# Performance work log

Measured on AMD Instinct MI355X. Metric: run time of the kernel, lower is better.

The kernel has to match this reference:

```python
import jax, jax.numpy as jnp
import numpy as np

K, D = 1024, 256
B, H, W = 32, 32, 32


def setup_inputs() -> dict:
    key = jax.random.key(0)
    kx, kc = jax.random.split(key)
    x = jax.random.normal(kx, (B, D, H, W), dtype=jnp.float32)
    # nn.Embedding weight initialized uniform(-1/K, 1/K)
    codebook = jax.random.uniform(kc, (K, D), dtype=jnp.float32,
                                  minval=-1.0 / K, maxval=1.0 / K)
    return {"x": x, "codebook": codebook}


def reference(x, codebook):
    # x: [B, D, H, W] -> NHWC -> flatten to [N, D]
    xf = jnp.transpose(x, (0, 2, 3, 1)).reshape(-1, D)  # [N, D]
    # Squared Euclidean distances via ||a||^2 - 2 a.b + ||b||^2.
    # torch.cdist applies sqrt; sqrt is monotone so argmin over squared
    # distances yields identical indices without the extra elementwise pass.
    x_sq = jnp.sum(xf * xf, axis=1, keepdims=True)          # [N, 1]
    e_sq = jnp.sum(codebook * codebook, axis=1)             # [K]
    d2 = x_sq - 2.0 * (xf @ codebook.T) + e_sq              # [N, K]
    indices = jnp.argmin(d2, axis=1)                        # [N]
    return indices.reshape(B, H, W)
```

## Files before the change

kernel.cpp:

```cpp
#include <hip/hip_runtime.h>

#define K_CODES 1024
#define DIMS    256
#define NROWS   32768

typedef __attribute__((ext_vector_type(8))) short bf16x8;
typedef __attribute__((ext_vector_type(4))) float f32x4;


#define WS_BH    0
#define WS_ESQ   (WS_BH + 131072)
#define WS_CAND  (WS_ESQ + K_CODES)
#define WS_XP    (WS_CAND + NROWS * 8)
#define WS_MFMA_NEED_FLOATS (WS_XP + 3 * NROWS)
#define WS_MFMA_NEED_BYTES  ((size_t)WS_MFMA_NEED_FLOATS * 4)

#define F32_ET    0
#define F32_ESQ   (F32_ET  + DIMS * K_CODES)
#define F32_XSQ   (F32_ESQ + K_CODES)
#define F32_CAND  (F32_XSQ + NROWS)
#define F32_NEED_FLOATS (F32_CAND + 4 * NROWS * 2)
#define F32_NEED_BYTES  ((size_t)F32_NEED_FLOATS * 4)

__device__ __forceinline__ float sq_at(const float* p, int d, int stride) {
#pragma clang fp contract(off)
    const float v = p[(size_t)d * stride];
    return v * v;
}

__device__ __forceinline__ float np_block_sq(const float* p, int stride, int o, int n) {
#pragma clang fp contract(off)
    float r[8];
    #pragma unroll
    for (int k = 0; k < 8; ++k) r[k] = sq_at(p, o + k, stride);
    const int n8 = n - (n % 8);
    for (int i = 8; i < n8; i += 8) {
        #pragma unroll
        for (int k = 0; k < 8; ++k) r[k] = r[k] + sq_at(p, o + i + k, stride);
    }
    float res = ((r[0] + r[1]) + (r[2] + r[3])) + ((r[4] + r[5]) + (r[6] + r[7]));
    for (int i = n8; i < n; ++i) res = res + sq_at(p, o + i, stride);
    return res;
}

__device__ __forceinline__ float np_sumsq_row(const float* p, int stride) {
#pragma clang fp contract(off)
    const float p120 = np_block_sq(p, stride, 1,   120);
    const float p64  = np_block_sq(p, stride, 121, 64);
    const float p71  = np_block_sq(p, stride, 185, 71);
    const float s135 = p64 + p71;
    const float s255 = p120 + s135;
    return sq_at(p, 0, stride) + s255;
}

__device__ __forceinline__ unsigned short f32_to_bf16_rne(float f) {
    unsigned u = __float_as_uint(f);
    u += 0x7fffu + ((u >> 16) & 1u);
    return (unsigned short)(u >> 16);
}

__global__ void vq_prologue_mfma(const float* __restrict__ x, const float* __restrict__ cb,
                                 float* __restrict__ esq, unsigned short* __restrict__ bh,
                                 float* __restrict__ xp) {
    const int bid = blockIdx.x;
    if (bid < 4) {
        const int c = bid * 256 + threadIdx.x;
        esq[c] = np_sumsq_row(cb + (size_t)c * DIMS, 1);
    } else if (bid < 1028) {
        const int idx = (bid - 4) * 256 + threadIdx.x;
        const int i  = idx & 7;
        const int ln = (idx >> 3) & 63;
        const int t  = (idx >> 9) & 63;
        const int kc = idx >> 15;
        const int c  = t * 16 + (ln & 15);
        const int k  = kc * 32 + (ln >> 4) * 8 + i;
        bh[idx] = f32_to_bf16_rne(cb[(size_t)c * DIMS + k]);
    } else {
        const int bid2  = bid - 1028;
        const int piece = bid2 / 128;
        const int n     = (bid2 % 128) * 256 + threadIdx.x;
        const float* p  = x + ((size_t)(n >> 10)) * (DIMS * 1024) + (n & 1023);
        const int o   = (piece == 0) ? 1   : (piece == 1) ? 121 : 185;
        const int len = (piece == 0) ? 120 : (piece == 1) ? 64  : 71;
        xp[(size_t)piece * NROWS + n] = np_block_sq(p, 1024, o, len);
    }
}

__global__ __launch_bounds__(256, 2)
void vq_mfma_filter(const float* __restrict__ x, const unsigned short* __restrict__ bh,
                    const float* __restrict__ esq, int4* __restrict__ cand) {
    __shared__ int4 lbh[2][1024];

    const int tid  = (int)threadIdx.x;
    const int wid  = __builtin_amdgcn_readfirstlane(tid >> 6);
    const int lane = tid & 63;
    const int h      = blockIdx.x & 1;
    const int rowblk = (blockIdx.x >> 1) * 4 + wid;
    const int row0 = rowblk * 16;
    const int b  = row0 >> 10;
    const int hw = (row0 & 1023) + (lane & 15);
    const float* xb = x + (size_t)b * (DIMS * 1024) + hw;
    const int g = lane >> 4;
    const int tile0 = h * 32;

    bf16x8 afr[8];
    #pragma unroll
    for (int kc = 0; kc < 8; ++kc) {
        #pragma unroll
        for (int i = 0; i < 8; ++i) {
            const int k = kc * 32 + g * 8 + i;
            afr[kc][i] = (short)f32_to_bf16_rne(xb[(size_t)k * 1024]);
        }
    }

    float lv[4][2]; int lc[4][2];
    #pragma unroll
    for (int j = 0; j < 4; ++j) {
        lv[j][0] = 3.4e38f; lv[j][1] = 3.4e38f;
        lc[j][0] = 0x7fffffff; lc[j][1] = 0x7fffffff;
    }

    const int4* bh4 = reinterpret_cast<const int4*>(bh);

#define STAGE(BUF, CHUNK)                                                      \
    do {                                                                       \
        _Pragma("unroll")                                                      \
        for (int e = 0; e < 4; ++e) {                                          \
            const int idx = e * 256 + tid;                        \
            const int ln_ = idx & 63;                                          \
            const int tt_ = (idx >> 6) & 1;                                    \
            const int kc_ = idx >> 7;                                          \
            lbh[BUF][idx] =                                                    \
                bh4[(kc_ * 64 + tile0 + (CHUNK) * 2 + tt_) * 64 + ln_];        \
        }                                                                      \
    } while (0)

    STAGE(0, 0);
    __syncthreads();
    for (int chunk = 0; chunk < 16; ++chunk) {
        const int cur = chunk & 1;
        if (chunk + 1 < 16) STAGE(cur ^ 1, chunk + 1);

        #pragma unroll
        for (int tt = 0; tt < 2; ++tt) {
            const int t = tile0 + chunk * 2 + tt;
            f32x4 acch = {0.f, 0.f, 0.f, 0.f};
            #pragma unroll
            for (int kc = 0; kc < 8; ++kc) {
                const int li = (kc * 2 + tt) * 64 + lane;
                acch = __builtin_amdgcn_mfma_f32_16x16x32_bf16(
                    afr[kc], *reinterpret_cast<const bf16x8*>(&lbh[cur][li]), acch, 0, 0, 0);
            }
            const int   c  = t * 16 + (lane & 15);
            const float es = esq[c];
            #pragma unroll
            for (int j = 0; j < 4; ++j) {
                const float v = fmaf(-2.0f, acch[j], es);
                if (v < lv[j][0]) { lv[j][1] = lv[j][0]; lc[j][1] = lc[j][0]; lv[j][0] = v; lc[j][0] = c; }
                else if (v < lv[j][1]) { lv[j][1] = v; lc[j][1] = c; }
            }
        }
        __syncthreads();
    }
#undef STAGE

    int c3[4][3];
    #pragma unroll
    for (int j = 0; j < 4; ++j) {
        float a1v = lv[j][0]; int a1c = lc[j][0];
        float a2v = lv[j][1]; int a2c = lc[j][1];
        #pragma unroll
        for (int e = 0; e < 3; ++e) {
            float mv = a1v; int mc = a1c;
            #pragma unroll
            for (int off = 1; off < 16; off <<= 1) {
                const float ov = __shfl_xor(mv, off, 16);
                const int   oc = __shfl_xor(mc, off, 16);
                if (ov < mv || (ov == mv && oc < mc)) { mv = ov; mc = oc; }
            }
            c3[j][e] = mc;
            if (a1c == mc) { a1v = a2v; a1c = a2c; a2v = 3.4e38f; a2c = 0x7fffffff; }
        }
    }
    if ((lane & 15) == 0) {
        #pragma unroll
        for (int j = 0; j < 4; ++j)
            cand[(size_t)h * NROWS + row0 + g * 4 + j] =
                make_int4(c3[j][0], c3[j][1], c3[j][2], 0);
    }
}

__global__ __launch_bounds__(192, 2)
void vq_refine_fused(const float* __restrict__ x, const float* __restrict__ cb,
                     const float* __restrict__ esq, const int4* __restrict__ cand,
                     const float* __restrict__ xp, int* __restrict__ out) {
    __shared__ float sacc[6][32];
    __shared__ int   scc[6][32];

    const int t    = (int)threadIdx.x;
    const int r    = t & 31;
    const int slot = t >> 5;
    const int n  = blockIdx.x * 32 + r;
    const int b  = n >> 10;
    const int hw = n & 1023;
    const float* xr = x + (size_t)b * (DIMS * 1024) + hw;

    const int4 cd = cand[(size_t)(slot / 3) * NROWS + n];
    const int k3 = slot % 3;
    const int cc = (k3 == 0) ? cd.x : (k3 == 1) ? cd.y : cd.z;

    float acc = 0.f;
    for (int d0 = 0; d0 < DIMS; d0 += 32) {
        float xv[32];
        #pragma unroll
        for (int i = 0; i < 32; ++i) xv[i] = xr[(size_t)(d0 + i) * 1024];
        const float4* ec4 = reinterpret_cast<const float4*>(cb + (size_t)cc * DIMS + d0);
        #pragma unroll
        for (int q = 0; q < 8; ++q) {
            const float4 e = ec4[q];
            acc = fmaf(xv[q * 4 + 0], e.x, acc);
            acc = fmaf(xv[q * 4 + 1], e.y, acc);
            acc = fmaf(xv[q * 4 + 2], e.z, acc);
            acc = fmaf(xv[q * 4 + 3], e.w, acc);
        }
    }
    sacc[slot][r] = acc;
    scc[slot][r]  = cc;
    __syncthreads();
    if (t < 32) {
#pragma clang fp contract(off)
        const int n2  = blockIdx.x * 32 + t;
        const float x0 = x[(size_t)(n2 >> 10) * (DIMS * 1024) + (n2 & 1023)];
        const float q0 = x0 * x0;
        const float p120 = xp[n2];
        const float p64  = xp[NROWS + n2];
        const float p71  = xp[2 * NROWS + n2];
        const float s135 = p64 + p71;
        const float s255 = p120 + s135;
        const float xs   = q0 + s255;
        float bestv = 3.4e38f; int bestc = 0x7fffffff;
        #pragma unroll
        for (int k = 0; k < 6; ++k) {
            const float t3 = xs - 2.0f * sacc[k][t];
            const float v  = t3 + esq[scc[k][t]];
            if (v < bestv || (v == bestv && scc[k][t] < bestc)) { bestv = v; bestc = scc[k][t]; }
        }
        out[n2] = bestc;
    }
}

__global__ void vq_prologue_f32(const float* __restrict__ x, const float* __restrict__ cb,
                                float* __restrict__ xsq, float* __restrict__ esq,
                                float4* __restrict__ et4) {
    const int bid = blockIdx.x;
    if (bid < 128) {
        const int n = bid * 256 + threadIdx.x;
        const float* p = x + ((size_t)(n >> 10)) * (DIMS * 1024) + (n & 1023);
        xsq[n] = np_sumsq_row(p, 1024);
    } else if (bid < 132) {
        const int c = (bid - 128) * 256 + threadIdx.x;
        esq[c] = np_sumsq_row(cb + (size_t)c * DIMS, 1);
    } else {
        const int idx = (bid - 132) * 256 + threadIdx.x;
        const int dk  = idx & 63;
        const int c   = idx >> 6;
        const float4 v = *reinterpret_cast<const float4*>(cb + (size_t)c * DIMS + dk * 4);
        et4[(size_t)dk * K_CODES + c] = v;
    }
}

__global__ __launch_bounds__(256, 2)
void vq_main7_kernel(const float* __restrict__ x, const float4* __restrict__ et4,
                     const float* __restrict__ esq, const float* __restrict__ xsq,
                     float2* __restrict__ cand) {
    const int wid  = __builtin_amdgcn_readfirstlane((int)(threadIdx.x >> 6));
    const int lane = threadIdx.x & 63;
    const int W     = blockIdx.x * 4 + wid;
    const int g     = W & 3;
    const int slice = W >> 2;
    const int c0    = g * 256 + lane;
    const int row_base = slice * 8;
    const int b    = row_base >> 10;
    const int hw0  = row_base & 1023;
    const float* xb = x + (size_t)b * (DIMS * 1024) + hw0;

    const float esq0 = esq[c0];
    const float esq1 = esq[c0 + 64];
    const float esq2 = esq[c0 + 128];
    const float esq3 = esq[c0 + 192];

    float acc0[8], acc1[8], acc2[8], acc3[8];
    #pragma unroll
    for (int r = 0; r < 8; ++r) { acc0[r] = 0.0f; acc1[r] = 0.0f; acc2[r] = 0.0f; acc3[r] = 0.0f; }

    for (int dk = 0; dk < DIMS / 4; ++dk) {
        const float4* ep = et4 + (size_t)dk * K_CODES;
        const float4 e0 = ep[c0];
        const float4 e1 = ep[c0 + 64];
        const float4 e2 = ep[c0 + 128];
        const float4 e3 = ep[c0 + 192];

        #pragma unroll
        for (int dd = 0; dd < 4; ++dd) {
            float xv[8];
            #pragma unroll
            for (int r = 0; r < 8; ++r)
                xv[r] = xb[(size_t)(dk * 4 + dd) * 1024 + r];
            const float ev0 = (dd == 0) ? e0.x : (dd == 1) ? e0.y : (dd == 2) ? e0.z : e0.w;
            const float ev1 = (dd == 0) ? e1.x : (dd == 1) ? e1.y : (dd == 2) ? e1.z : e1.w;
            const float ev2 = (dd == 0) ? e2.x : (dd == 1) ? e2.y : (dd == 2) ? e2.z : e2.w;
            const float ev3 = (dd == 0) ? e3.x : (dd == 1) ? e3.y : (dd == 2) ? e3.z : e3.w;
            #pragma unroll
            for (int r = 0; r < 8; ++r) acc0[r] = fmaf(xv[r], ev0, acc0[r]);
            #pragma unroll
            for (int r = 0; r < 8; ++r) acc1[r] = fmaf(xv[r], ev1, acc1[r]);
            #pragma unroll
            for (int r = 0; r < 8; ++r) acc2[r] = fmaf(xv[r], ev2, acc2[r]);
            #pragma unroll
            for (int r = 0; r < 8; ++r) acc3[r] = fmaf(xv[r], ev3, acc3[r]);
        }
    }

    {
#pragma clang fp contract(off)
        float keepv = 0.0f; int keepc = 0;
        #pragma unroll
        for (int r = 0; r < 8; ++r) {
            const float xs_r = xsq[row_base + r];
            const float v0 = (xs_r - 2.0f * acc0[r]) + esq0;
            const float v1 = (xs_r - 2.0f * acc1[r]) + esq1;
            const float v2 = (xs_r - 2.0f * acc2[r]) + esq2;
            const float v3 = (xs_r - 2.0f * acc3[r]) + esq3;
            float bv = v0; int bc = c0;
            if (v1 < bv) { bv = v1; bc = c0 + 64; }
            if (v2 < bv) { bv = v2; bc = c0 + 128; }
            if (v3 < bv) { bv = v3; bc = c0 + 192; }
            #pragma unroll
            for (int off = 1; off < 64; off <<= 1) {
                const float ov = __shfl_xor(bv, off, 64);
                const int   oc = __shfl_xor(bc, off, 64);
                if (ov < bv || (ov == bv && oc < bc)) { bv = ov; bc = oc; }
            }
            if (lane == r) { keepv = bv; keepc = bc; }
        }
        if (lane < 8) {
            cand[(size_t)g * NROWS + row_base + lane] =
                make_float2(keepv, __int_as_float(keepc));
        }
    }
}

__global__ void vq_reduce_kernel(const float2* __restrict__ cand, int* __restrict__ out) {
    const int row = blockIdx.x * 256 + threadIdx.x;
    float2 p = cand[row];
    float bv = p.x; int bc = __float_as_int(p.y);
    #pragma unroll
    for (int gg = 1; gg < 4; ++gg) {
        const float2 q = cand[(size_t)gg * NROWS + row];
        const float v = q.x; const int qc = __float_as_int(q.y);
        if (v < bv || (v == bv && qc < bc)) { bv = v; bc = qc; }
    }
    out[row] = bc;
}

extern "C" void kernel_launch(void* const* d_in, const int* in_sizes, int n_in,
                              void* d_out, int out_size, void* d_ws, size_t ws_size,
                              hipStream_t stream) {
    const float* x  = (const float*)d_in[0];
    const float* cb = (const float*)d_in[1];
    int* out = (int*)d_out;
    float* ws = (float*)d_ws;

    if (ws_size >= WS_MFMA_NEED_BYTES) {
        unsigned short* bh = (unsigned short*)(ws + WS_BH);
        float* esq = ws + WS_ESQ;
        int4*  cnd = (int4*)(ws + WS_CAND);
        float* xp  = ws + WS_XP;

        vq_prologue_mfma<<<4 + 1024 + 384, 256, 0, stream>>>(x, cb, esq, bh, xp);
        vq_mfma_filter<<<1024, 256, 0, stream>>>(x, bh, esq, cnd);
        vq_refine_fused<<<NROWS / 32, 192, 0, stream>>>(x, cb, esq, cnd, xp, out);
        return;
    }
    {
        float4* et4  = (float4*)(ws + F32_ET);
        float*  esq  = ws + F32_ESQ;
        float*  xsq  = ws + F32_XSQ;
        float2* cand = (float2*)(ws + F32_CAND);

        vq_prologue_f32<<<128 + 4 + 256, 256, 0, stream>>>(x, cb, xsq, esq, et4);
        vq_main7_kernel<<<(NROWS / 8) * 4 / 4, 256, 0, stream>>>(x, et4, esq, xsq, cand);
        vq_reduce_kernel<<<NROWS / 256, 256, 0, stream>>>(cand, out);
    }
}
```

Measured before the change: 95.75 us.

## Split codebook into quarters, process two row groups per wave, keep top-2 candidates

The MFMA filter now gives each wave 32 rows (two 16-row A fragments) and a quarter of the codebook, so every staged B fragment from LDS feeds two MFMAs and codebook staging traffic per row is halved. Each quarter keeps top-2 candidates instead of each half keeping top-3, giving 8 candidates per row for the exact fp32 refine instead of 6. The refine kernel grows to 256 threads to rescore the 8 candidates. This raises register pressure in the filter (two A fragment sets and two accumulators) and increases refine work, while the candidate coverage changes and may affect correctness near ties.

```diff
diff --git a/kernel.cpp b/kernel.cpp
--- a/kernel.cpp
+++ b/kernel.cpp
@@ -88,37 +88,41 @@
 
 __global__ __launch_bounds__(256, 2)
 void vq_mfma_filter(const float* __restrict__ x, const unsigned short* __restrict__ bh,
-                    const float* __restrict__ esq, int4* __restrict__ cand) {
+                    const float* __restrict__ esq, int2* __restrict__ cand) {
     __shared__ int4 lbh[2][1024];
 
     const int tid  = (int)threadIdx.x;
     const int wid  = __builtin_amdgcn_readfirstlane(tid >> 6);
     const int lane = tid & 63;
-    const int h      = blockIdx.x & 1;
-    const int rowblk = (blockIdx.x >> 1) * 4 + wid;
-    const int row0 = rowblk * 16;
+    const int q      = blockIdx.x & 3;
+    const int rowblk = (blockIdx.x >> 2) * 4 + wid;
+    const int row0 = rowblk * 32;
     const int b  = row0 >> 10;
     const int hw = (row0 & 1023) + (lane & 15);
-    const float* xb = x + (size_t)b * (DIMS * 1024) + hw;
+    const float* xb0 = x + (size_t)b * (DIMS * 1024) + hw;
+    const float* xb1 = xb0 + 16;
     const int g = lane >> 4;
-    const int tile0 = h * 32;
-
-    bf16x8 afr[8];
+    const int tile0 = q * 16;
+
+    bf16x8 afr0[8], afr1[8];
     #pragma unroll
     for (int kc = 0; kc < 8; ++kc) {
         #pragma unroll
         for (int i = 0; i < 8; ++i) {
             const int k = kc * 32 + g * 8 + i;
-            afr[kc][i] = (short)f32_to_bf16_rne(xb[(size_t)k * 1024]);
-        }
-    }
-
-    float lv[4][2]; int lc[4][2];
-    #pragma unroll
-    for (int j = 0; j < 4; ++j) {
-        lv[j][0] = 3.4e38f; lv[j][1] = 3.4e38f;
-        lc[j][0] = 0x7fffffff; lc[j][1] = 0x7fffffff;
-    }
+            afr0[kc][i] = (short)f32_to_bf16_rne(xb0[(size_t)k * 1024]);
+            afr1[kc][i] = (short)f32_to_bf16_rne(xb1[(size_t)k * 1024]);
+        }
+    }
+
+    float lv[2][4][2]; int lc[2][4][2];
+    #pragma unroll
+    for (int rg = 0; rg < 2; ++rg)
+        #pragma unroll
+        for (int j = 0; j < 4; ++j) {
+            lv[rg][j][0] = 3.4e38f; lv[rg][j][1] = 3.4e38f;
+            lc[rg][j][0] = 0x7fffffff; lc[rg][j][1] = 0x7fffffff;
+        }
 
     const int4* bh4 = reinterpret_cast<const int4*>(bh);
 
@@ -137,65 +141,73 @@
 
     STAGE(0, 0);
     __syncthreads();
-    for (int chunk = 0; chunk < 16; ++chunk) {
+    for (int chunk = 0; chunk < 8; ++chunk) {
         const int cur = chunk & 1;
-        if (chunk + 1 < 16) STAGE(cur ^ 1, chunk + 1);
+        if (chunk + 1 < 8) STAGE(cur ^ 1, chunk + 1);
 
         #pragma unroll
         for (int tt = 0; tt < 2; ++tt) {
             const int t = tile0 + chunk * 2 + tt;
-            f32x4 acch = {0.f, 0.f, 0.f, 0.f};
+            f32x4 acc0 = {0.f, 0.f, 0.f, 0.f};
+            f32x4 acc1 = {0.f, 0.f, 0.f, 0.f};
             #pragma unroll
             for (int kc = 0; kc < 8; ++kc) {
                 const int li = (kc * 2 + tt) * 64 + lane;
-                acch = __builtin_amdgcn_mfma_f32_16x16x32_bf16(
-                    afr[kc], *reinterpret_cast<const bf16x8*>(&lbh[cur][li]), acch, 0, 0, 0);
+                const bf16x8 bf = *reinterpret_cast<const bf16x8*>(&lbh[cur][li]);
+                acc0 = __builtin_amdgcn_mfma_f32_16x16x32_bf16(afr0[kc], bf, acc0, 0, 0, 0);
+                acc1 = __builtin_amdgcn_mfma_f32_16x16x32_bf16(afr1[kc], bf, acc1, 0, 0, 0);
             }
             const int   c  = t * 16 + (lane & 15);
             const float es = esq[c];
             #pragma unroll
             for (int j = 0; j < 4; ++j) {
-                const float v = fmaf(-2.0f, acch[j], es);
-                if (v < lv[j][0]) { lv[j][1] = lv[j][0]; lc[j][1] = lc[j][0]; lv[j][0] = v; lc[j][0] = c; }
-                else if (v < lv[j][1]) { lv[j][1] = v; lc[j][1] = c; }
+                const float v0 = fmaf(-2.0f, acc0[j], es);
+                if (v0 < lv[0][j][0]) { lv[0][j][1] = lv[0][j][0]; lc[0][j][1] = lc[0][j][0]; lv[0][j][0] = v0; lc[0][j][0] = c; }
+                else if (v0 < lv[0][j][1]) { lv[0][j][1] = v0; lc[0][j][1] = c; }
+                const float v1 = fmaf(-2.0f, acc1[j], es);
+                if (v1 < lv[1][j][0]) { lv[1][j][1] = lv[1][j][0]; lc[1][j][1] = lc[1][j][0]; lv[1][j][0] = v1; lc[1][j][0] = c; }
+                else if (v1 < lv[1][j][1]) { lv[1][j][1] = v1; lc[1][j][1] = c; }
             }
         }
         __syncthreads();
     }
 #undef STAGE
 
-    int c3[4][3];
-    #pragma unroll
-    for (int j = 0; j < 4; ++j) {
-        float a1v = lv[j][0]; int a1c = lc[j][0];
-        float a2v = lv[j][1]; int a2c = lc[j][1];
-        #pragma unroll
-        for (int e = 0; e < 3; ++e) {
-            float mv = a1v; int mc = a1c;
-            #pragma unroll
-            for (int off = 1; off < 16; off <<= 1) {
-                const float ov = __shfl_xor(mv, off, 16);
-                const int   oc = __shfl_xor(mc, off, 16);
-                if (ov < mv || (ov == mv && oc < mc)) { mv = ov; mc = oc; }
+    #pragma unroll
+    for (int rg = 0; rg < 2; ++rg) {
+        int c2[4][2];
+        #pragma unroll
+        for (int j = 0; j < 4; ++j) {
+            float a1v = lv[rg][j][0]; int a1c = lc[rg][j][0];
+            float a2v = lv[rg][j][1]; int a2c = lc[rg][j][1];
+            #pragma unroll
+            for (int e = 0; e < 2; ++e) {
+                float mv = a1v; int mc = a1c;
+                #pragma unroll
+                for (int off = 1; off < 16; off <<= 1) {
+                    const float ov = __shfl_xor(mv, off, 16);
+                    const int   oc = __shfl_xor(mc, off, 16);
+                    if (ov < mv || (ov == mv && oc < mc)) { mv = ov; mc = oc; }
+                }
+                c2[j][e] = mc;
+                if (a1c == mc) { a1v = a2v; a1c = a2c; a2v = 3.4e38f; a2c = 0x7fffffff; }
             }
-            c3[j][e] = mc;
-            if (a1c == mc) { a1v = a2v; a1c = a2c; a2v = 3.4e38f; a2c = 0x7fffffff; }
-        }
-    }
-    if ((lane & 15) == 0) {
-        #pragma unroll
-        for (int j = 0; j < 4; ++j)
-            cand[(size_t)h * NROWS + row0 + g * 4 + j] =
-                make_int4(c3[j][0], c3[j][1], c3[j][2], 0);
-    }
-}
-
-__global__ __launch_bounds__(192, 2)
+        }
+        if ((lane & 15) == 0) {
+            #pragma unroll
+            for (int j = 0; j < 4; ++j)
+                cand[(size_t)q * NROWS + row0 + rg * 16 + g * 4 + j] =
+                    make_int2(c2[j][0], c2[j][1]);
+        }
+    }
+}
+
+__global__ __launch_bounds__(256, 2)
 void vq_refine_fused(const float* __restrict__ x, const float* __restrict__ cb,
-                     const float* __restrict__ esq, const int4* __restrict__ cand,
+                     const float* __restrict__ esq, const int2* __restrict__ cand,
                      const float* __restrict__ xp, int* __restrict__ out) {
-    __shared__ float sacc[6][32];
-    __shared__ int   scc[6][32];
+    __shared__ float sacc[8][32];
+    __shared__ int   scc[8][32];
 
     const int t    = (int)threadIdx.x;
     const int r    = t & 31;
@@ -205,9 +217,8 @@
     const int hw = n & 1023;
     const float* xr = x + (size_t)b * (DIMS * 1024) + hw;
 
-    const int4 cd = cand[(size_t)(slot / 3) * NROWS + n];
-    const int k3 = slot % 3;
-    const int cc = (k3 == 0) ? cd.x : (k3 == 1) ? cd.y : cd.z;
+    const int2 cd = cand[(size_t)(slot >> 1) * NROWS + n];
+    const int cc = (slot & 1) ? cd.y : cd.x;
 
     float acc = 0.f;
     for (int d0 = 0; d0 < DIMS; d0 += 32) {
@@ -216,12 +227,12 @@
         for (int i = 0; i < 32; ++i) xv[i] = xr[(size_t)(d0 + i) * 1024];
         const float4* ec4 = reinterpret_cast<const float4*>(cb + (size_t)cc * DIMS + d0);
         #pragma unroll
-        for (int q = 0; q < 8; ++q) {
-            const float4 e = ec4[q];
-            acc = fmaf(xv[q * 4 + 0], e.x, acc);
-            acc = fmaf(xv[q * 4 + 1], e.y, acc);
-            acc = fmaf(xv[q * 4 + 2], e.z, acc);
-            acc = fmaf(xv[q * 4 + 3], e.w, acc);
+        for (int qq = 0; qq < 8; ++qq) {
+            const float4 e = ec4[qq];
+            acc = fmaf(xv[qq * 4 + 0], e.x, acc);
+            acc = fmaf(xv[qq * 4 + 1], e.y, acc);
+            acc = fmaf(xv[qq * 4 + 2], e.z, acc);
+            acc = fmaf(xv[qq * 4 + 3], e.w, acc);
         }
     }
     sacc[slot][r] = acc;
@@ -240,7 +251,7 @@
         const float xs   = q0 + s255;
         float bestv = 3.4e38f; int bestc = 0x7fffffff;
         #pragma unroll
-        for (int k = 0; k < 6; ++k) {
+        for (int k = 0; k < 8; ++k) {
             const float t3 = xs - 2.0f * sacc[k][t];
             const float v  = t3 + esq[scc[k][t]];
             if (v < bestv || (v == bestv && scc[k][t] < bestc)) { bestv = v; bestc = scc[k][t]; }
@@ -374,12 +385,12 @@
     if (ws_size >= WS_MFMA_NEED_BYTES) {
         unsigned short* bh = (unsigned short*)(ws + WS_BH);
         float* esq = ws + WS_ESQ;
-        int4*  cnd = (int4*)(ws + WS_CAND);
+        int2*  cnd = (int2*)(ws + WS_CAND);
         float* xp  = ws + WS_XP;
 
         vq_prologue_mfma<<<4 + 1024 + 384, 256, 0, stream>>>(x, cb, esq, bh, xp);
         vq_mfma_filter<<<1024, 256, 0, stream>>>(x, bh, esq, cnd);
-        vq_refine_fused<<<NROWS / 32, 192, 0, stream>>>(x, cb, esq, cnd, xp, out);
+        vq_refine_fused<<<NROWS / 32, 256, 0, stream>>>(x, cb, esq, cnd, xp, out);
         return;
     }
     {
```

New measurement: 114.3 us. 19.3% more time.

## Switch filter kernel to 32x32x16 bf16 MFMA tiles with 32-row waves

Applied to the files above, without the earlier changes.

The filter kernel moves from 16x16x32 MFMA to 32x32x16 MFMA. Each wave now covers 32 rows instead of 16, and each tile covers 32 codes. The codebook bf16 layout and the LDS staging are reorganized to match, and the block count is halved. The larger tile reuses each A and B fragment over more outputs per instruction, lowering LDS traffic per flop. In exchange it raises register pressure (16 A fragments, 16x2 top-2 trackers, a 16-float accumulator) and lengthens the cross-lane reductions to 32 lanes.

```diff
diff --git a/kernel.cpp b/kernel.cpp
--- a/kernel.cpp
+++ b/kernel.cpp
@@ -4,8 +4,8 @@
 #define DIMS    256
 #define NROWS   32768
 
-typedef __attribute__((ext_vector_type(8))) short bf16x8;
-typedef __attribute__((ext_vector_type(4))) float f32x4;
+typedef __attribute__((ext_vector_type(8)))  short bf16x8;
+typedef __attribute__((ext_vector_type(16))) float f32x16;
 
 
 #define WS_BH    0
@@ -68,12 +68,12 @@
         esq[c] = np_sumsq_row(cb + (size_t)c * DIMS, 1);
     } else if (bid < 1028) {
         const int idx = (bid - 4) * 256 + threadIdx.x;
-        const int i  = idx & 7;
-        const int ln = (idx >> 3) & 63;
-        const int t  = (idx >> 9) & 63;
-        const int kc = idx >> 15;
-        const int c  = t * 16 + (ln & 15);
-        const int k  = kc * 32 + (ln >> 4) * 8 + i;
+        const int i    = idx & 7;
+        const int ln   = (idx >> 3) & 63;
+        const int tile = (idx >> 9) & 31;
+        const int kc   = idx >> 14;
+        const int c = tile * 32 + (ln & 31);
+        const int k = kc * 16 + (ln >> 5) * 8 + i;
         bh[idx] = f32_to_bf16_rne(cb[(size_t)c * DIMS + k]);
     } else {
         const int bid2  = bid - 1028;
@@ -96,97 +96,89 @@
     const int lane = tid & 63;
     const int h      = blockIdx.x & 1;
     const int rowblk = (blockIdx.x >> 1) * 4 + wid;
-    const int row0 = rowblk * 16;
+    const int row0 = rowblk * 32;
     const int b  = row0 >> 10;
-    const int hw = (row0 & 1023) + (lane & 15);
+    const int hw = (row0 & 1023) + (lane & 31);
     const float* xb = x + (size_t)b * (DIMS * 1024) + hw;
-    const int g = lane >> 4;
-    const int tile0 = h * 32;
-
-    bf16x8 afr[8];
-    #pragma unroll
-    for (int kc = 0; kc < 8; ++kc) {
+    const int tile0 = h * 16;
+
+    bf16x8 afr[16];
+    #pragma unroll
+    for (int kc = 0; kc < 16; ++kc) {
         #pragma unroll
         for (int i = 0; i < 8; ++i) {
-            const int k = kc * 32 + g * 8 + i;
+            const int k = kc * 16 + (lane >> 5) * 8 + i;
             afr[kc][i] = (short)f32_to_bf16_rne(xb[(size_t)k * 1024]);
         }
     }
 
-    float lv[4][2]; int lc[4][2];
-    #pragma unroll
-    for (int j = 0; j < 4; ++j) {
-        lv[j][0] = 3.4e38f; lv[j][1] = 3.4e38f;
-        lc[j][0] = 0x7fffffff; lc[j][1] = 0x7fffffff;
+    float lv[16][2]; int lc[16][2];
+    #pragma unroll
+    for (int r = 0; r < 16; ++r) {
+        lv[r][0] = 3.4e38f; lv[r][1] = 3.4e38f;
+        lc[r][0] = 0x7fffffff; lc[r][1] = 0x7fffffff;
     }
 
     const int4* bh4 = reinterpret_cast<const int4*>(bh);
 
-#define STAGE(BUF, CHUNK)                                                      \
+#define STAGE(BUF, TILE)                                                       \
     do {                                                                       \
         _Pragma("unroll")                                                      \
         for (int e = 0; e < 4; ++e) {                                          \
             const int idx = e * 256 + tid;                        \
             const int ln_ = idx & 63;                                          \
-            const int tt_ = (idx >> 6) & 1;                                    \
-            const int kc_ = idx >> 7;                                          \
-            lbh[BUF][idx] =                                                    \
-                bh4[(kc_ * 64 + tile0 + (CHUNK) * 2 + tt_) * 64 + ln_];        \
+            const int kc_ = idx >> 6;                               \
+            lbh[BUF][idx] = bh4[(kc_ * 32 + (TILE)) * 64 + ln_];               \
         }                                                                      \
     } while (0)
 
-    STAGE(0, 0);
+    STAGE(0, tile0);
     __syncthreads();
-    for (int chunk = 0; chunk < 16; ++chunk) {
-        const int cur = chunk & 1;
-        if (chunk + 1 < 16) STAGE(cur ^ 1, chunk + 1);
-
-        #pragma unroll
-        for (int tt = 0; tt < 2; ++tt) {
-            const int t = tile0 + chunk * 2 + tt;
-            f32x4 acch = {0.f, 0.f, 0.f, 0.f};
-            #pragma unroll
-            for (int kc = 0; kc < 8; ++kc) {
-                const int li = (kc * 2 + tt) * 64 + lane;
-                acch = __builtin_amdgcn_mfma_f32_16x16x32_bf16(
-                    afr[kc], *reinterpret_cast<const bf16x8*>(&lbh[cur][li]), acch, 0, 0, 0);
-            }
-            const int   c  = t * 16 + (lane & 15);
-            const float es = esq[c];
-            #pragma unroll
-            for (int j = 0; j < 4; ++j) {
-                const float v = fmaf(-2.0f, acch[j], es);
-                if (v < lv[j][0]) { lv[j][1] = lv[j][0]; lc[j][1] = lc[j][0]; lv[j][0] = v; lc[j][0] = c; }
-                else if (v < lv[j][1]) { lv[j][1] = v; lc[j][1] = c; }
-            }
+    for (int t = 0; t < 16; ++t) {
+        const int cur = t & 1;
+        if (t + 1 < 16) STAGE(cur ^ 1, tile0 + t + 1);
+
+        f32x16 acc = {0.f, 0.f, 0.f, 0.f, 0.f, 0.f, 0.f, 0.f,
+                      0.f, 0.f, 0.f, 0.f, 0.f, 0.f, 0.f, 0.f};
+        #pragma unroll
+        for (int kc = 0; kc < 16; ++kc) {
+            const int li = kc * 64 + lane;
+            acc = __builtin_amdgcn_mfma_f32_32x32x16_bf16(
+                afr[kc], *reinterpret_cast<const bf16x8*>(&lbh[cur][li]), acc, 0, 0, 0);
+        }
+        const int   c  = (tile0 + t) * 32 + (lane & 31);
+        const float es = esq[c];
+        #pragma unroll
+        for (int r = 0; r < 16; ++r) {
+            const float v = fmaf(-2.0f, acc[r], es);
+            if (v < lv[r][0]) { lv[r][1] = lv[r][0]; lc[r][1] = lc[r][0]; lv[r][0] = v; lc[r][0] = c; }
+            else if (v < lv[r][1]) { lv[r][1] = v; lc[r][1] = c; }
         }
         __syncthreads();
     }
 #undef STAGE
 
-    int c3[4][3];
-    #pragma unroll
-    for (int j = 0; j < 4; ++j) {
-        float a1v = lv[j][0]; int a1c = lc[j][0];
-        float a2v = lv[j][1]; int a2c = lc[j][1];
+    #pragma unroll
+    for (int r = 0; r < 16; ++r) {
+        float a1v = lv[r][0]; int a1c = lc[r][0];
+        float a2v = lv[r][1]; int a2c = lc[r][1];
+        int c3[3];
         #pragma unroll
         for (int e = 0; e < 3; ++e) {
             float mv = a1v; int mc = a1c;
             #pragma unroll
-            for (int off = 1; off < 16; off <<= 1) {
-                const float ov = __shfl_xor(mv, off, 16);
-                const int   oc = __shfl_xor(mc, off, 16);
+            for (int off = 1; off < 32; off <<= 1) {
+                const float ov = __shfl_xor(mv, off, 64);
+                const int   oc = __shfl_xor(mc, off, 64);
                 if (ov < mv || (ov == mv && oc < mc)) { mv = ov; mc = oc; }
             }
-            c3[j][e] = mc;
+            c3[e] = mc;
             if (a1c == mc) { a1v = a2v; a1c = a2c; a2v = 3.4e38f; a2c = 0x7fffffff; }
         }
-    }
-    if ((lane & 15) == 0) {
-        #pragma unroll
-        for (int j = 0; j < 4; ++j)
-            cand[(size_t)h * NROWS + row0 + g * 4 + j] =
-                make_int4(c3[j][0], c3[j][1], c3[j][2], 0);
+        if ((lane & 31) == 0) {
+            const int R = row0 + (r & 3) + 8 * (r >> 2) + 4 * (lane >> 5);
+            cand[(size_t)h * NROWS + R] = make_int4(c3[0], c3[1], c3[2], 0);
+        }
     }
 }
 
@@ -378,7 +370,7 @@
         float* xp  = ws + WS_XP;
 
         vq_prologue_mfma<<<4 + 1024 + 384, 256, 0, stream>>>(x, cb, esq, bh, xp);
-        vq_mfma_filter<<<1024, 256, 0, stream>>>(x, bh, esq, cnd);
+        vq_mfma_filter<<<512, 256, 0, stream>>>(x, bh, esq, cnd);
         vq_refine_fused<<<NROWS / 32, 192, 0, stream>>>(x, cb, esq, cnd, xp, out);
         return;
     }
```

New measurement: 119.1 us. 24.4% more time.
